# Kernel optimization log

Hardware: AMD Instinct MI355X
Metric: run time of the kernel (lower is better)

The kernel has to match this reference:

```python
import jax, jax.numpy as jnp
import numpy as np

B, N, S, C1, C2 = 8, 8192, 2048, 128, 256
IN_CH = C1 + C2
MLP = [256, 128]
EPS_INTERP = 1e-8
EPS_BN = 1e-5


def setup_inputs() -> dict:
    key = jax.random.key(0)
    ks = jax.random.split(key, 8)
    inp = {
        "xyz1": jax.random.normal(ks[0], (B, 3, N), dtype=jnp.float32),
        "xyz2": jax.random.normal(ks[1], (B, 3, S), dtype=jnp.float32),
        "points1": jax.random.normal(ks[2], (B, C1, N), dtype=jnp.float32),
        "points2": jax.random.normal(ks[3], (B, C2, S), dtype=jnp.float32),
        # Conv1d(k=1) weights as [out, in] matrices, plus BN gamma/beta
        "W1": jax.random.normal(ks[4], (MLP[0], IN_CH), dtype=jnp.float32) * 0.02,
        "b1": jnp.zeros((MLP[0],), dtype=jnp.float32),
        "g1": jnp.ones((MLP[0],), dtype=jnp.float32),
        "be1": jnp.zeros((MLP[0],), dtype=jnp.float32),
        "W2": jax.random.normal(ks[5], (MLP[1], MLP[0]), dtype=jnp.float32) * 0.02,
        "b2": jnp.zeros((MLP[1],), dtype=jnp.float32),
        "g2": jnp.ones((MLP[1],), dtype=jnp.float32),
        "be2": jnp.zeros((MLP[1],), dtype=jnp.float32),
    }
    return inp


def _conv_bn_relu(x, W, b, g, be):
    # x: [B, N, Cin]; 1x1 Conv1d == per-point matmul; BN over (batch, length) per channel (training-mode stats)
    y = jnp.einsum('bnc,oc->bno', x, W) + b
    m = jnp.mean(y, axis=(0, 1))
    v = jnp.var(y, axis=(0, 1))
    return jax.nn.relu((y - m) * jax.lax.rsqrt(v + EPS_BN) * g + be)


def reference(xyz1, xyz2, points1, points2, W1, b1, g1, be1, W2, b2, g2, be2):
    x1 = xyz1.transpose(0, 2, 1)   # [B, N, 3]
    x2 = xyz2.transpose(0, 2, 1)   # [B, S, 3]
    p2 = points2.transpose(0, 2, 1)  # [B, S, C2]
    p1 = points1.transpose(0, 2, 1)  # [B, N, C1]

    # squared pairwise distances [B, N, S]
    d = (jnp.sum(x1 * x1, axis=-1, keepdims=True)
         - 2.0 * jnp.einsum('bnd,bsd->bns', x1, x2)
         + jnp.sum(x2 * x2, axis=-1)[:, None, :])

    # 3 nearest neighbors (smallest distances)
    neg_d, idx = jax.lax.top_k(-d, 3)          # idx: [B, N, 3]
    d3 = -neg_d                                 # [B, N, 3]
    recip = 1.0 / (d3 + EPS_INTERP)
    w = recip / jnp.sum(recip, axis=-1, keepdims=True)  # [B, N, 3]

    gathered = jax.vmap(lambda p, i: p[i])(p2, idx)     # [B, N, 3, C2]
    interp = jnp.sum(gathered * w[..., None], axis=2)   # [B, N, C2]

    x = jnp.concatenate([p1, interp], axis=-1)          # [B, N, C1+C2]
    x = _conv_bn_relu(x, W1, b1, g1, be1)
    x = _conv_bn_relu(x, W2, b2, g2, be2)
    return x.transpose(0, 2, 1)                         # [B, mlp[-1], N]
```

## Files before the change

### kernel.cpp

```cpp
#include <hip/hip_runtime.h>
#include <stdint.h>

#define B_ 8
#define N_ 8192
#define S_ 2048
#define C1_ 128
#define C2_ 256
#define IN_ 384
#define H1_ 256
#define H2_ 128
#define M_ (B_*N_)

typedef short bf16x8 __attribute__((ext_vector_type(8)));
typedef float f32x4 __attribute__((ext_vector_type(4)));

__device__ __forceinline__ float bf2f(unsigned short s){
  union { unsigned int u; float f; } x; x.u = ((unsigned int)s) << 16; return x.f;
}
__device__ __forceinline__ unsigned short f2bf(float f){
  union { float f; unsigned int u; } x; x.f = f;
  unsigned int u = x.u;
  unsigned int r = (u + 0x7FFFu + ((u >> 16) & 1u)) >> 16;
  return (unsigned short)r;
}

__device__ __forceinline__ size_t fragaddr(int m, int k, int K){
  return ((size_t)((m >> 4) * (K >> 5) + (k >> 5)) << 9)
       + (size_t)((((k >> 3) & 3) << 7) + ((m & 15) << 3) + (k & 7));
}

__device__ __forceinline__ void gload_lds16(const unsigned short* g, unsigned short* l){
  __builtin_amdgcn_global_load_lds(
      (const __attribute__((address_space(1))) unsigned int*)g,
      (__attribute__((address_space(3))) unsigned int*)l, 16, 0, 0);
}

#define PIECES_ 8
#define SPP_ (S_ / PIECES_)

__device__ __forceinline__ void insert_k(float& k0, float& k1, float& k2, float x){
  k2 = __builtin_amdgcn_fmed3f(k1, k2, x);
  k1 = __builtin_amdgcn_fmed3f(k0, k1, x);
  k0 = fminf(k0, x);
}

__device__ __forceinline__ void insert3(float& d0, float& d1, float& d2,
                                        int& i0, int& i1, int& i2,
                                        float x, int s){
  bool b0 = x < d0, b1 = x < d1, b2 = x < d2;
  i2 = b1 ? i1 : (b2 ? s : i2);
  i1 = b0 ? i0 : (b1 ? s : i1);
  i0 = b0 ? s : i0;
  d2 = __builtin_amdgcn_fmed3f(d1, d2, x);
  d1 = __builtin_amdgcn_fmed3f(d0, d1, x);
  d0 = fminf(d0, x);
}

__global__ __launch_bounds__(256) void prep_knn_fused(
    const float* W1, const float* W2, const float* p2, const float* p1,
    const float* xyz1, const float* xyz2,
    unsigned short* w1b, unsigned short* w2b, float* stats,
    unsigned short* p2t, unsigned short* x,
    float* partd, int* parti)
{
  __shared__ __align__(16) char smraw[4224];
  float (*tile)[33] = reinterpret_cast<float(*)[33]>(smraw);
  float4* pts = reinterpret_cast<float4*>(smraw);

  const int per = blockIdx.x / 115;
  const int r   = blockIdx.x % 115;
  const int t   = threadIdx.x;

  if (r < 16){
    int kid = per*16 + r;
    int nb = kid & 31, b = (kid >> 5) & 7, piece = kid >> 8;
    int n = nb*256 + t;
    int base = piece * SPP_;
    const float* x2 = xyz2 + (size_t)b * 3 * S_;
    {
      float px = x2[base + t], py = x2[S_ + base + t], pz = x2[2*S_ + base + t];
      pts[t] = make_float4(-2.f*px, -2.f*py, -2.f*pz, px*px + py*py + pz*pz);
    }
    __syncthreads();
    const float* x1 = xyz1 + (size_t)b * 3 * N_;
    float ax = x1[n], ay = x1[N_ + n], az = x1[2*N_ + n];
    float x1sq = ax*ax + ay*ay + az*az;

    const float KINIT = __uint_as_float(0x7F000000u);
    float k[2][3];
    k[0][0]=k[0][1]=k[0][2]=KINIT;
    k[1][0]=k[1][1]=k[1][2]=KINIT;

    for (int s = 0; s < SPP_; s += 8){
      #pragma unroll
      for (int u = 0; u < 8; u++){
        float4 c = pts[s + u];
        float dd = fmaf(ax, c.x, fmaf(ay, c.y, fmaf(az, c.z, c.w + x1sq)));
        float key = __uint_as_float((__float_as_uint(dd) & 0xFFFFFF00u) | (unsigned)(s + u));
        int L = u & 1;
        insert_k(k[L][0], k[L][1], k[L][2], key);
      }
    }
    float e0 = k[0][0], e1 = k[0][1], e2 = k[0][2];
    insert_k(e0, e1, e2, k[1][0]);
    insert_k(e0, e1, e2, k[1][1]);
    insert_k(e0, e1, e2, k[1][2]);

    float ed[3]; int ei[3];
    float ev[3] = {e0, e1, e2};
    #pragma unroll
    for (int j = 0; j < 3; j++){
      int li = (int)(__float_as_uint(ev[j]) & 0xFFu);
      float4 c = pts[li];
      float dd = fmaf(ax, c.x, fmaf(ay, c.y, fmaf(az, c.z, c.w + x1sq)));
      ed[j] = fmaxf(dd, 0.f);
      ei[j] = base + li;
    }

    size_t g = (size_t)b * N_ + n;
    partd[(piece*3 + 0)*(size_t)M_ + g] = ed[0];
    partd[(piece*3 + 1)*(size_t)M_ + g] = ed[1];
    partd[(piece*3 + 2)*(size_t)M_ + g] = ed[2];
    parti[(piece*3 + 0)*(size_t)M_ + g] = ei[0];
    parti[(piece*3 + 1)*(size_t)M_ + g] = ei[1];
    parti[(piece*3 + 2)*(size_t)M_ + g] = ei[2];
    return;
  }

  const int pid = per*99 + (r - 16);
  if (pid < 384){
    int i = pid * 256 + t;
    if (i < 256*384){
      int row = i / 384, col = i - row*384;
      w1b[fragaddr(row, col, 384)] = f2bf(W1[i]);
    }
    if (i < 128*256){
      int row = i >> 8, col = i & 255;
      w2b[fragaddr(row, col, 256)] = f2bf(W2[i]);
    }
    if (i < 1536) stats[i] = 0.f;
    return;
  }
  int tx = t & 31, ty = t >> 5;
  if (pid < 4480){
    int id = pid - 384;
    int b = id >> 9, rem = id & 511;
    int l0 = (rem & 63) * 32, r0 = (rem >> 6) * 32;
    const float* src = p2 + (size_t)b * C2_ * S_;
    #pragma unroll
    for (int rr = ty; rr < 32; rr += 8)
      tile[rr][tx] = src[(size_t)(r0 + rr) * S_ + l0 + tx];
    __syncthreads();
    unsigned short* dst = p2t + (size_t)b * S_ * C2_;
    #pragma unroll
    for (int rr = ty; rr < 32; rr += 8)
      dst[(size_t)(l0 + rr) * C2_ + r0 + tx] = f2bf(tile[tx][rr]);
    return;
  }
  {
    int id = pid - 4480;
    int b = id >> 10, rem = id & 1023;
    int l0 = (rem & 255) * 32, r0 = (rem >> 8) * 32;
    const float* src = p1 + (size_t)b * C1_ * N_;
    #pragma unroll
    for (int rr = ty; rr < 32; rr += 8)
      tile[rr][tx] = src[(size_t)(r0 + rr) * N_ + l0 + tx];
    __syncthreads();
    #pragma unroll
    for (int rr = ty; rr < 32; rr += 8){
      int g = b * N_ + l0 + rr;
      size_t a = ((size_t)((g >> 4)*12 + (r0 >> 5)) << 9)
               + (size_t)((((tx >> 3) & 3) << 7) + ((g & 15) << 3) + (tx & 7));
      x[a] = f2bf(tile[tx][rr]);
    }
  }
}

__global__ __launch_bounds__(256) void interp_kernel(const float* partd, const int* parti,
                                                     const unsigned short* p2t, unsigned short* x){
  __shared__ int   sidx[16][3];
  __shared__ float swgt[16][3];
  int t = threadIdx.x;
  int base = blockIdx.x * 16;
  if (t < 16){
    size_t g = (size_t)base + t;
    float d0 = partd[0*(size_t)M_ + g], d1 = partd[1*(size_t)M_ + g], d2 = partd[2*(size_t)M_ + g];
    int   i0 = parti[0*(size_t)M_ + g], i1 = parti[1*(size_t)M_ + g], i2 = parti[2*(size_t)M_ + g];
    #pragma unroll
    for (int p = 1; p < PIECES_; p++)
      #pragma unroll
      for (int j = 0; j < 3; j++)
        insert3(d0, d1, d2, i0, i1, i2,
                partd[(p*3 + j)*(size_t)M_ + g], parti[(p*3 + j)*(size_t)M_ + g]);
    float r0 = 1.f/(d0 + 1e-8f), r1 = 1.f/(d1 + 1e-8f), r2 = 1.f/(d2 + 1e-8f);
    float rs = 1.f/(r0 + r1 + r2);
    sidx[t][0] = i0; sidx[t][1] = i1; sidx[t][2] = i2;
    swgt[t][0] = r0*rs; swgt[t][1] = r1*rs; swgt[t][2] = r2*rs;
  }
  __syncthreads();
  size_t suboff = (size_t)((((t >> 3) & 3) << 7) + (t & 7));
  for (int k = 0; k < 16; k++){
    int g = base + k;
    int b = g >> 13;
    const unsigned short* p = p2t + (size_t)b * S_ * C2_;
    float v = swgt[k][0]*bf2f(p[(size_t)sidx[k][0]*C2_ + t])
            + swgt[k][1]*bf2f(p[(size_t)sidx[k][1]*C2_ + t])
            + swgt[k][2]*bf2f(p[(size_t)sidx[k][2]*C2_ + t]);
    size_t a = ((size_t)((g >> 4)*12 + 4 + (t >> 5)) << 9) + suboff + (size_t)((g & 15) << 3);
    x[a] = f2bf(v);
  }
}

__device__ __forceinline__ bf16x8 bn_relu_frag(bf16x8 v, const float* a, const float* c, int kb){
  union { bf16x8 h; unsigned short s[8]; } u; u.h = v;
  union { float4 v4; float f[4]; } a0, a1, c0, c1;
  a0.v4 = *(const float4*)(a + kb);  a1.v4 = *(const float4*)(a + kb + 4);
  c0.v4 = *(const float4*)(c + kb);  c1.v4 = *(const float4*)(c + kb + 4);
  #pragma unroll
  for (int j = 0; j < 4; j++){
    float f0 = fmaf(a0.f[j], bf2f(u.s[j]),     c0.f[j]);
    float f1 = fmaf(a1.f[j], bf2f(u.s[j + 4]), c1.f[j]);
    u.s[j]     = f2bf(fmaxf(f0, 0.f));
    u.s[j + 4] = f2bf(fmaxf(f1, 0.f));
  }
  return u.h;
}

template<int K, bool HAS_AFF, bool OUT_FRAG>
__global__ __launch_bounds__(256) void gemm_lds_kernel(
    const unsigned short* __restrict__ A, const unsigned short* __restrict__ Wf,
    unsigned short* __restrict__ Cout, int Ntot,
    float* pbuf, const float* aff_a, const float* aff_c)
{
  constexpr int KT = K / 32;
  __shared__ unsigned short smA[128*64];
  __shared__ unsigned short smB[128*64];
  __shared__ float ldsStat[256];

  const int t = threadIdx.x;
  const int lane = t & 63, wave = t >> 6;
  const int ln = lane & 15, lq = lane >> 4;
  const int wm = wave >> 1, wn = wave & 1;
  const int mtb = blockIdx.x * 8;
  const int ntb = blockIdx.y * 8;
  const int mtw = mtb + wm * 4;
  const int n0  = blockIdx.y * 128 + wn * 64;

  ldsStat[t] = 0.f;

  const int c0 = 2*wave, c1 = 2*wave + 1;

  const f32x4 fzero = {0.f, 0.f, 0.f, 0.f};
  f32x4 acc[4][4];
  #pragma unroll
  for (int i = 0; i < 4; i++)
    #pragma unroll
    for (int j = 0; j < 4; j++) acc[i][j] = fzero;

  for (int kk = 0; kk < KT; kk += 2){
    #pragma unroll
    for (int q = 0; q < 2; q++){
      gload_lds16(A  + (((size_t)((mtb + c0)*KT + kk + q)) << 9) + lane*8,
                  &smA[((c0*2 + q) << 9) + lane*8]);
      gload_lds16(A  + (((size_t)((mtb + c1)*KT + kk + q)) << 9) + lane*8,
                  &smA[((c1*2 + q) << 9) + lane*8]);
      gload_lds16(Wf + (((size_t)((ntb + c0)*KT + kk + q)) << 9) + lane*8,
                  &smB[((c0*2 + q) << 9) + lane*8]);
      gload_lds16(Wf + (((size_t)((ntb + c1)*KT + kk + q)) << 9) + lane*8,
                  &smB[((c1*2 + q) << 9) + lane*8]);
    }
    __syncthreads();
    #pragma unroll
    for (int q = 0; q < 2; q++){
      bf16x8 af[4], bfr[4];
      #pragma unroll
      for (int i = 0; i < 4; i++)
        af[i] = *(const bf16x8*)(&smA[(((wm*4 + i)*2 + q) << 9) + lane*8]);
      #pragma unroll
      for (int j = 0; j < 4; j++)
        bfr[j] = *(const bf16x8*)(&smB[(((wn*4 + j)*2 + q) << 9) + lane*8]);
      if (HAS_AFF){
        const int kb = (kk + q)*32 + lq*8;
        #pragma unroll
        for (int i = 0; i < 4; i++) af[i] = bn_relu_frag(af[i], aff_a, aff_c, kb);
      }
      #pragma unroll
      for (int i = 0; i < 4; i++)
        #pragma unroll
        for (int j = 0; j < 4; j++)
          acc[i][j] = __builtin_amdgcn_mfma_f32_16x16x32_bf16(af[i], bfr[j], acc[i][j], 0, 0, 0);
    }
    __syncthreads();
  }

  #pragma unroll
  for (int j = 0; j < 4; j++){
    int ncol = n0 + j*16 + ln;
    float s = 0.f, q = 0.f;
    #pragma unroll
    for (int i = 0; i < 4; i++){
      #pragma unroll
      for (int r = 0; r < 4; r++){
        float v = acc[i][j][r];
        if (OUT_FRAG){
          size_t a = ((size_t)((mtw + i)*8 + (ncol >> 5)) << 9)
                   + (size_t)((((ncol >> 3) & 3) << 7) + ((lq*4 + r) << 3) + (ncol & 7));
          Cout[a] = f2bf(v);
        } else {
          Cout[((size_t)((mtw + i)*16 + lq*4 + r)) * Ntot + ncol] = f2bf(v);
        }
        s += v; q += v*v;
      }
    }
    s += __shfl_xor(s, 16); s += __shfl_xor(s, 32);
    q += __shfl_xor(q, 16); q += __shfl_xor(q, 32);
    if (lq == 0){
      int colLocal = wn*64 + j*16 + ln;
      atomicAdd(&ldsStat[colLocal], s);
      atomicAdd(&ldsStat[128 + colLocal], q);
    }
  }
  __syncthreads();
  pbuf[((size_t)(blockIdx.y * gridDim.x + blockIdx.x) << 8) + t] = ldsStat[t];
}

__global__ __launch_bounds__(256) void finalize_kernel(const float* pbuf, const float* g,
                                                       const float* be, float* a_out,
                                                       float* c_out){
  __shared__ float red[8];
  int c = blockIdx.x, t = threadIdx.x;
  int grp = c >> 7, lc = c & 127;
  const float* base = pbuf + ((size_t)(grp * 512) << 8);
  float s = base[((size_t)t << 8) + lc]       + base[((size_t)(t + 256) << 8) + lc];
  float q = base[((size_t)t << 8) + 128 + lc] + base[((size_t)(t + 256) << 8) + 128 + lc];
  #pragma unroll
  for (int o = 1; o < 64; o <<= 1){ s += __shfl_xor(s, o); q += __shfl_xor(q, o); }
  int w = t >> 6;
  if ((t & 63) == 0){ red[w] = s; red[4 + w] = q; }
  __syncthreads();
  if (t == 0){
    s = red[0] + red[1] + red[2] + red[3];
    q = red[4] + red[5] + red[6] + red[7];
    float mean = s * (1.f / M_);
    float var  = q * (1.f / M_) - mean*mean;
    float a = g[c] * rsqrtf(var + 1e-5f);
    a_out[c] = a;
    c_out[c] = fmaf(-mean, a, be[c]);
  }
}

__global__ __launch_bounds__(256) void out_kernel(const unsigned short* y2, const float* a2,
                                                  const float* c2, float* out){
  __shared__ float lds[64][65];
  int t  = threadIdx.x;
  int b  = blockIdx.z;
  int n0 = blockIdx.y * 64;
  int c0 = blockIdx.x * 64;
  int cc = t & 63, tr = t >> 6;
  float a = a2[c0 + cc], cadd = c2[c0 + cc];
  #pragma unroll
  for (int ph = 0; ph < 16; ph++){
    int nr = tr + ph*4;
    unsigned short v = y2[((size_t)(b*N_ + n0 + nr)) * H2_ + c0 + cc];
    lds[nr][cc] = fmaxf(fmaf(a, bf2f(v), cadd), 0.f);
  }
  __syncthreads();
  #pragma unroll
  for (int ph = 0; ph < 16; ph++){
    int cr = tr + ph*4;
    out[((size_t)(b*H2_ + c0 + cr)) * N_ + n0 + cc] = lds[cc][cr];
  }
}

extern "C" void kernel_launch(void* const* d_in, const int* in_sizes, int n_in,
                              void* d_out, int out_size, void* d_ws, size_t ws_size,
                              hipStream_t stream){
  const float* xyz1 = (const float*)d_in[0];
  const float* xyz2 = (const float*)d_in[1];
  const float* p1   = (const float*)d_in[2];
  const float* p2   = (const float*)d_in[3];
  const float* W1   = (const float*)d_in[4];
  const float* g1   = (const float*)d_in[6];
  const float* be1  = (const float*)d_in[7];
  const float* W2   = (const float*)d_in[8];
  const float* g2   = (const float*)d_in[10];
  const float* be2  = (const float*)d_in[11];
  float* out = (float*)d_out;

  char* ws = (char*)d_ws;
  unsigned short* x    = (unsigned short*)(ws + 0);
  unsigned short* p2t  = (unsigned short*)(ws + 50331648);
  unsigned short* y1   = (unsigned short*)(ws + 58720256);
  unsigned short* y2   = (unsigned short*)(ws + 92274688);
  unsigned short* w1b  = (unsigned short*)(ws + 109051904);
  unsigned short* w2b  = (unsigned short*)(ws + 109248512);
  float*          stats= (float*)(ws + 110886912);
  float* a1   = stats + 768;  float* c1  = stats + 1024;
  float* a2   = stats + 1280; float* c2  = stats + 1408;
  float* partd = (float*)y1;
  int*   parti = (int*)(y1 + 6291456);
  float* pbuf1 = (float*)p2t;
  float* pbuf2 = (float*)x;

  prep_knn_fused<<<14720, 256, 0, stream>>>(W1, W2, p2, p1, xyz1, xyz2,
                                            w1b, w2b, stats, p2t, x, partd, parti);
  interp_kernel<<<4096, 256, 0, stream>>>(partd, parti, p2t, x);
  gemm_lds_kernel<384, false, true><<<dim3(512, 2), 256, 0, stream>>>(
      x, w1b, y1, 256, pbuf1, nullptr, nullptr);
  finalize_kernel<<<256, 256, 0, stream>>>(pbuf1, g1, be1, a1, c1);
  gemm_lds_kernel<256, true, false><<<dim3(512, 1), 256, 0, stream>>>(
      y1, w2b, y2, 128, pbuf2, a1, c1);
  finalize_kernel<<<128, 256, 0, stream>>>(pbuf2, g2, be2, a2, c2);
  out_kernel<<<dim3(2, 128, 8), 256, 0, stream>>>(y2, a2, c2, out);
}
```

Before: 242.3 us.

## Merge KNN pieces in-block and fuse interpolation with points1 transpose

Each KNN block now walks all S pieces in sequence, staging every piece in LDS. It merges the per-piece top-3 in registers and writes final indices and inverse-distance weights directly, removing the partial distance/index buffers and the separate merge pass. Interpolation and the points1 transpose into the GEMM input layout move into a new build kernel, and the p2 transpose now shares a kernel with KNN and the weight conversion. The aim is to cut global traffic and one launch. The cost is far fewer KNN blocks (one per 256 query points), each serialising all pieces with extra barriers, which lowers parallelism on that stage. The stats zeroing is also dropped.

```diff
diff --git a/kernel.cpp b/kernel.cpp
--- a/kernel.cpp
+++ b/kernel.cpp
@@ -56,96 +56,92 @@
   d0 = fminf(d0, x);
 }
 
-__global__ __launch_bounds__(256) void prep_knn_fused(
-    const float* W1, const float* W2, const float* p2, const float* p1,
+__global__ __launch_bounds__(256) void p2t_knn_kernel(
+    const float* W1, const float* W2, const float* p2,
     const float* xyz1, const float* xyz2,
-    unsigned short* w1b, unsigned short* w2b, float* stats,
-    unsigned short* p2t, unsigned short* x,
-    float* partd, int* parti)
+    unsigned short* w1b, unsigned short* w2b,
+    unsigned short* p2t, int* ibuf, float* wbuf)
 {
-  __shared__ __align__(16) char smraw[4224];
+  __shared__ __align__(16) char smraw[4352];
   float (*tile)[33] = reinterpret_cast<float(*)[33]>(smraw);
   float4* pts = reinterpret_cast<float4*>(smraw);
-
-  const int per = blockIdx.x / 115;
-  const int r   = blockIdx.x % 115;
-  const int t   = threadIdx.x;
-
-  if (r < 16){
-    int kid = per*16 + r;
-    int nb = kid & 31, b = (kid >> 5) & 7, piece = kid >> 8;
-    int n = nb*256 + t;
-    int base = piece * SPP_;
+  const int bx = blockIdx.x, t = threadIdx.x;
+
+  if (bx >= 4352){
+    int i = (bx - 4352) * 256 + t;
+    if (i < 256*384){
+      int row = i / 384, col = i - row*384;
+      w1b[fragaddr(row, col, 384)] = f2bf(W1[i]);
+    }
+    if (i < 128*256){
+      int row = i >> 8, col = i & 255;
+      w2b[fragaddr(row, col, 256)] = f2bf(W2[i]);
+    }
+    return;
+  }
+
+  const int per = bx / 17, r = bx % 17;
+  if (r == 0){
+    int kid = per;
+    int b = kid >> 5, nb = kid & 31;
+    int n = nb * 256 + t;
     const float* x2 = xyz2 + (size_t)b * 3 * S_;
-    {
-      float px = x2[base + t], py = x2[S_ + base + t], pz = x2[2*S_ + base + t];
-      pts[t] = make_float4(-2.f*px, -2.f*py, -2.f*pz, px*px + py*py + pz*pz);
-    }
-    __syncthreads();
     const float* x1 = xyz1 + (size_t)b * 3 * N_;
     float ax = x1[n], ay = x1[N_ + n], az = x1[2*N_ + n];
     float x1sq = ax*ax + ay*ay + az*az;
 
     const float KINIT = __uint_as_float(0x7F000000u);
-    float k[2][3];
-    k[0][0]=k[0][1]=k[0][2]=KINIT;
-    k[1][0]=k[1][1]=k[1][2]=KINIT;
-
-    for (int s = 0; s < SPP_; s += 8){
+    float gd0 = KINIT, gd1 = KINIT, gd2 = KINIT;
+    int   gi0 = 0,     gi1 = 0,     gi2 = 0;
+
+    for (int p = 0; p < PIECES_; p++){
+      int base = p * SPP_;
+      __syncthreads();
+      {
+        float px = x2[base + t], py = x2[S_ + base + t], pz = x2[2*S_ + base + t];
+        pts[t] = make_float4(-2.f*px, -2.f*py, -2.f*pz, px*px + py*py + pz*pz);
+      }
+      __syncthreads();
+      float ka[3] = {KINIT, KINIT, KINIT};
+      float kb[3] = {KINIT, KINIT, KINIT};
+      for (int s = 0; s < SPP_; s += 8){
+        float4 cb[8];
+        #pragma unroll
+        for (int u = 0; u < 8; u++) cb[u] = pts[s + u];
+        #pragma unroll
+        for (int u = 0; u < 8; u++){
+          float dd = fmaf(ax, cb[u].x, fmaf(ay, cb[u].y, fmaf(az, cb[u].z, cb[u].w + x1sq)));
+          float key = __uint_as_float((__float_as_uint(dd) & 0xFFFFFF00u) | (unsigned)(s + u));
+          if (u & 1) insert_k(kb[0], kb[1], kb[2], key);
+          else       insert_k(ka[0], ka[1], ka[2], key);
+        }
+      }
+      insert_k(ka[0], ka[1], ka[2], kb[0]);
+      insert_k(ka[0], ka[1], ka[2], kb[1]);
+      insert_k(ka[0], ka[1], ka[2], kb[2]);
       #pragma unroll
-      for (int u = 0; u < 8; u++){
-        float4 c = pts[s + u];
+      for (int j = 0; j < 3; j++){
+        int li = (int)(__float_as_uint(ka[j]) & 0xFFu);
+        float4 c = pts[li];
         float dd = fmaf(ax, c.x, fmaf(ay, c.y, fmaf(az, c.z, c.w + x1sq)));
-        float key = __uint_as_float((__float_as_uint(dd) & 0xFFFFFF00u) | (unsigned)(s + u));
-        int L = u & 1;
-        insert_k(k[L][0], k[L][1], k[L][2], key);
-      }
-    }
-    float e0 = k[0][0], e1 = k[0][1], e2 = k[0][2];
-    insert_k(e0, e1, e2, k[1][0]);
-    insert_k(e0, e1, e2, k[1][1]);
-    insert_k(e0, e1, e2, k[1][2]);
-
-    float ed[3]; int ei[3];
-    float ev[3] = {e0, e1, e2};
-    #pragma unroll
-    for (int j = 0; j < 3; j++){
-      int li = (int)(__float_as_uint(ev[j]) & 0xFFu);
-      float4 c = pts[li];
-      float dd = fmaf(ax, c.x, fmaf(ay, c.y, fmaf(az, c.z, c.w + x1sq)));
-      ed[j] = fmaxf(dd, 0.f);
-      ei[j] = base + li;
-    }
-
+        dd = fmaxf(dd, 0.f);
+        insert3(gd0, gd1, gd2, gi0, gi1, gi2, dd, base + li);
+      }
+    }
+
+    float r0 = 1.f/(gd0 + 1e-8f), r1 = 1.f/(gd1 + 1e-8f), r2 = 1.f/(gd2 + 1e-8f);
+    float rs = 1.f/(r0 + r1 + r2);
     size_t g = (size_t)b * N_ + n;
-    partd[(piece*3 + 0)*(size_t)M_ + g] = ed[0];
-    partd[(piece*3 + 1)*(size_t)M_ + g] = ed[1];
-    partd[(piece*3 + 2)*(size_t)M_ + g] = ed[2];
-    parti[(piece*3 + 0)*(size_t)M_ + g] = ei[0];
-    parti[(piece*3 + 1)*(size_t)M_ + g] = ei[1];
-    parti[(piece*3 + 2)*(size_t)M_ + g] = ei[2];
+    ibuf[0*(size_t)M_ + g] = gi0; ibuf[1*(size_t)M_ + g] = gi1; ibuf[2*(size_t)M_ + g] = gi2;
+    wbuf[0*(size_t)M_ + g] = r0*rs; wbuf[1*(size_t)M_ + g] = r1*rs; wbuf[2*(size_t)M_ + g] = r2*rs;
     return;
   }
 
-  const int pid = per*99 + (r - 16);
-  if (pid < 384){
-    int i = pid * 256 + t;
-    if (i < 256*384){
-      int row = i / 384, col = i - row*384;
-      w1b[fragaddr(row, col, 384)] = f2bf(W1[i]);
-    }
-    if (i < 128*256){
-      int row = i >> 8, col = i & 255;
-      w2b[fragaddr(row, col, 256)] = f2bf(W2[i]);
-    }
-    if (i < 1536) stats[i] = 0.f;
-    return;
-  }
-  int tx = t & 31, ty = t >> 5;
-  if (pid < 4480){
-    int id = pid - 384;
-    int b = id >> 9, rem = id & 511;
+  {
+    int pid = per*16 + (r - 1);
+    int b = pid >> 9, rem = pid & 511;
     int l0 = (rem & 63) * 32, r0 = (rem >> 6) * 32;
+    int tx = t & 31, ty = t >> 5;
     const float* src = p2 + (size_t)b * C2_ * S_;
     #pragma unroll
     for (int rr = ty; rr < 32; rr += 8)
@@ -155,12 +151,49 @@
     #pragma unroll
     for (int rr = ty; rr < 32; rr += 8)
       dst[(size_t)(l0 + rr) * C2_ + r0 + tx] = f2bf(tile[tx][rr]);
+  }
+}
+
+__global__ __launch_bounds__(256) void xbuild_kernel(
+    const float* p1, const unsigned short* p2t,
+    const int* ibuf, const float* wbuf, unsigned short* x)
+{
+  __shared__ __align__(16) char smraw[4352];
+  float (*tile)[33] = reinterpret_cast<float(*)[33]>(smraw);
+  int*   sidx = reinterpret_cast<int*>(smraw);
+  float* swgt = reinterpret_cast<float*>(smraw + 192);
+  const int bx = blockIdx.x, t = threadIdx.x;
+  const int per = bx / 3, r = bx % 3;
+
+  if (r == 0){
+    int base = per * 16;
+    if (t < 64){
+      int q = t >> 2, j = t & 3;
+      if (j < 3){
+        sidx[q*3 + j] = ibuf[(size_t)j*M_ + base + q];
+        swgt[q*3 + j] = wbuf[(size_t)j*M_ + base + q];
+      }
+    }
+    __syncthreads();
+    size_t suboff = (size_t)((((t >> 3) & 3) << 7) + (t & 7));
+    for (int k = 0; k < 16; k++){
+      int g = base + k;
+      int b = g >> 13;
+      const unsigned short* p = p2t + (size_t)b * S_ * C2_;
+      float v = swgt[k*3+0]*bf2f(p[(size_t)sidx[k*3+0]*C2_ + t])
+              + swgt[k*3+1]*bf2f(p[(size_t)sidx[k*3+1]*C2_ + t])
+              + swgt[k*3+2]*bf2f(p[(size_t)sidx[k*3+2]*C2_ + t]);
+      size_t a = ((size_t)((g >> 4)*12 + 4 + (t >> 5)) << 9) + suboff + (size_t)((g & 15) << 3);
+      x[a] = f2bf(v);
+    }
     return;
   }
+
   {
-    int id = pid - 4480;
-    int b = id >> 10, rem = id & 1023;
+    int pid = per*2 + (r - 1);
+    int b = pid >> 10, rem = pid & 1023;
     int l0 = (rem & 255) * 32, r0 = (rem >> 8) * 32;
+    int tx = t & 31, ty = t >> 5;
     const float* src = p1 + (size_t)b * C1_ * N_;
     #pragma unroll
     for (int rr = ty; rr < 32; rr += 8)
@@ -173,41 +206,6 @@
                + (size_t)((((tx >> 3) & 3) << 7) + ((g & 15) << 3) + (tx & 7));
       x[a] = f2bf(tile[tx][rr]);
     }
-  }
-}
-
-__global__ __launch_bounds__(256) void interp_kernel(const float* partd, const int* parti,
-                                                     const unsigned short* p2t, unsigned short* x){
-  __shared__ int   sidx[16][3];
-  __shared__ float swgt[16][3];
-  int t = threadIdx.x;
-  int base = blockIdx.x * 16;
-  if (t < 16){
-    size_t g = (size_t)base + t;
-    float d0 = partd[0*(size_t)M_ + g], d1 = partd[1*(size_t)M_ + g], d2 = partd[2*(size_t)M_ + g];
-    int   i0 = parti[0*(size_t)M_ + g], i1 = parti[1*(size_t)M_ + g], i2 = parti[2*(size_t)M_ + g];
-    #pragma unroll
-    for (int p = 1; p < PIECES_; p++)
-      #pragma unroll
-      for (int j = 0; j < 3; j++)
-        insert3(d0, d1, d2, i0, i1, i2,
-                partd[(p*3 + j)*(size_t)M_ + g], parti[(p*3 + j)*(size_t)M_ + g]);
-    float r0 = 1.f/(d0 + 1e-8f), r1 = 1.f/(d1 + 1e-8f), r2 = 1.f/(d2 + 1e-8f);
-    float rs = 1.f/(r0 + r1 + r2);
-    sidx[t][0] = i0; sidx[t][1] = i1; sidx[t][2] = i2;
-    swgt[t][0] = r0*rs; swgt[t][1] = r1*rs; swgt[t][2] = r2*rs;
-  }
-  __syncthreads();
-  size_t suboff = (size_t)((((t >> 3) & 3) << 7) + (t & 7));
-  for (int k = 0; k < 16; k++){
-    int g = base + k;
-    int b = g >> 13;
-    const unsigned short* p = p2t + (size_t)b * S_ * C2_;
-    float v = swgt[k][0]*bf2f(p[(size_t)sidx[k][0]*C2_ + t])
-            + swgt[k][1]*bf2f(p[(size_t)sidx[k][1]*C2_ + t])
-            + swgt[k][2]*bf2f(p[(size_t)sidx[k][2]*C2_ + t]);
-    size_t a = ((size_t)((g >> 4)*12 + 4 + (t >> 5)) << 9) + suboff + (size_t)((g & 15) << 3);
-    x[a] = f2bf(v);
   }
 }
 
@@ -397,14 +395,13 @@
   float*          stats= (float*)(ws + 110886912);
   float* a1   = stats + 768;  float* c1  = stats + 1024;
   float* a2   = stats + 1280; float* c2  = stats + 1408;
-  float* partd = (float*)y1;
-  int*   parti = (int*)(y1 + 6291456);
+  int*   ibuf = (int*)y1;
+  float* wbuf = (float*)(ws + 58720256 + 0x100000);
   float* pbuf1 = (float*)p2t;
   float* pbuf2 = (float*)x;
 
-  prep_knn_fused<<<14720, 256, 0, stream>>>(W1, W2, p2, p1, xyz1, xyz2,
-                                            w1b, w2b, stats, p2t, x, partd, parti);
-  interp_kernel<<<4096, 256, 0, stream>>>(partd, parti, p2t, x);
+  p2t_knn_kernel<<<4736, 256, 0, stream>>>(W1, W2, p2, xyz1, xyz2, w1b, w2b, p2t, ibuf, wbuf);
+  xbuild_kernel<<<12288, 256, 0, stream>>>(p1, p2t, ibuf, wbuf, x);
   gemm_lds_kernel<384, false, true><<<dim3(512, 2), 256, 0, stream>>>(
       x, w1b, y1, 256, pbuf1, nullptr, nullptr);
   finalize_kernel<<<256, 256, 0, stream>>>(pbuf1, g1, be1, a1, c1);
```

New measurement: 294.3 us. +21.5%, slower.

## Split interpolation into parallel merge kernel and vectorized gather kernel

Applied to the files above, without the earlier changes.

The combined interp kernel merged per-piece top-3 candidates using only 16 threads per block, so 240 of 256 threads sat idle during the merge. The merge now runs as its own kernel with one thread per point and writes indices and weights to a workspace buffer. A separate gather kernel loads 4 bf16 channels per lane with vector loads, puts one wave on each point, and writes 8-byte stores. This costs an extra kernel launch and a round trip of the index and weight arrays through global memory.

```diff
diff --git a/kernel.cpp b/kernel.cpp
--- a/kernel.cpp
+++ b/kernel.cpp
@@ -13,6 +13,8 @@
 
 typedef short bf16x8 __attribute__((ext_vector_type(8)));
 typedef float f32x4 __attribute__((ext_vector_type(4)));
+typedef short short4v __attribute__((ext_vector_type(4)));
+typedef unsigned short ushort4v __attribute__((ext_vector_type(4)));
 
 __device__ __forceinline__ float bf2f(unsigned short s){
   union { unsigned int u; float f; } x; x.u = ((unsigned int)s) << 16; return x.f;
@@ -176,38 +178,64 @@
   }
 }
 
-__global__ __launch_bounds__(256) void interp_kernel(const float* partd, const int* parti,
-                                                     const unsigned short* p2t, unsigned short* x){
-  __shared__ int   sidx[16][3];
-  __shared__ float swgt[16][3];
-  int t = threadIdx.x;
+__global__ __launch_bounds__(256) void merge_kernel(const float* __restrict__ partd,
+                                                    const int* __restrict__ parti,
+                                                    int* __restrict__ ibuf,
+                                                    float* __restrict__ wbuf){
+  size_t g = (size_t)blockIdx.x * 256 + threadIdx.x;
+  float d0 = partd[0*(size_t)M_ + g], d1 = partd[1*(size_t)M_ + g], d2 = partd[2*(size_t)M_ + g];
+  int   i0 = parti[0*(size_t)M_ + g], i1 = parti[1*(size_t)M_ + g], i2 = parti[2*(size_t)M_ + g];
+  #pragma unroll
+  for (int p = 1; p < PIECES_; p++)
+    #pragma unroll
+    for (int j = 0; j < 3; j++)
+      insert3(d0, d1, d2, i0, i1, i2,
+              partd[(p*3 + j)*(size_t)M_ + g], parti[(p*3 + j)*(size_t)M_ + g]);
+  float r0 = 1.f/(d0 + 1e-8f), r1 = 1.f/(d1 + 1e-8f), r2 = 1.f/(d2 + 1e-8f);
+  float rs = 1.f/(r0 + r1 + r2);
+  ibuf[0*(size_t)M_ + g] = i0;    ibuf[1*(size_t)M_ + g] = i1;    ibuf[2*(size_t)M_ + g] = i2;
+  wbuf[0*(size_t)M_ + g] = r0*rs; wbuf[1*(size_t)M_ + g] = r1*rs; wbuf[2*(size_t)M_ + g] = r2*rs;
+}
+
+__global__ __launch_bounds__(256) void gather_kernel(
+    const unsigned short* __restrict__ p2t, const int* __restrict__ ibuf,
+    const float* __restrict__ wbuf, unsigned short* __restrict__ x)
+{
+  __shared__ int   sidx[48];
+  __shared__ float swgt[48];
+  const int t = threadIdx.x;
   int base = blockIdx.x * 16;
-  if (t < 16){
-    size_t g = (size_t)base + t;
-    float d0 = partd[0*(size_t)M_ + g], d1 = partd[1*(size_t)M_ + g], d2 = partd[2*(size_t)M_ + g];
-    int   i0 = parti[0*(size_t)M_ + g], i1 = parti[1*(size_t)M_ + g], i2 = parti[2*(size_t)M_ + g];
-    #pragma unroll
-    for (int p = 1; p < PIECES_; p++)
-      #pragma unroll
-      for (int j = 0; j < 3; j++)
-        insert3(d0, d1, d2, i0, i1, i2,
-                partd[(p*3 + j)*(size_t)M_ + g], parti[(p*3 + j)*(size_t)M_ + g]);
-    float r0 = 1.f/(d0 + 1e-8f), r1 = 1.f/(d1 + 1e-8f), r2 = 1.f/(d2 + 1e-8f);
-    float rs = 1.f/(r0 + r1 + r2);
-    sidx[t][0] = i0; sidx[t][1] = i1; sidx[t][2] = i2;
-    swgt[t][0] = r0*rs; swgt[t][1] = r1*rs; swgt[t][2] = r2*rs;
+  if (t < 64){
+    int q = t >> 2, j = t & 3;
+    if (j < 3){
+      sidx[q*3 + j] = ibuf[(size_t)j*M_ + base + q];
+      swgt[q*3 + j] = wbuf[(size_t)j*M_ + base + q];
+    }
   }
   __syncthreads();
-  size_t suboff = (size_t)((((t >> 3) & 3) << 7) + (t & 7));
-  for (int k = 0; k < 16; k++){
+  const int wv = t >> 6, ln = t & 63;
+  #pragma unroll
+  for (int kq = 0; kq < 4; kq++){
+    int k = kq*4 + wv;
     int g = base + k;
     int b = g >> 13;
     const unsigned short* p = p2t + (size_t)b * S_ * C2_;
-    float v = swgt[k][0]*bf2f(p[(size_t)sidx[k][0]*C2_ + t])
-            + swgt[k][1]*bf2f(p[(size_t)sidx[k][1]*C2_ + t])
-            + swgt[k][2]*bf2f(p[(size_t)sidx[k][2]*C2_ + t]);
-    size_t a = ((size_t)((g >> 4)*12 + 4 + (t >> 5)) << 9) + suboff + (size_t)((g & 15) << 3);
-    x[a] = f2bf(v);
+    float a0 = 0.f, a1 = 0.f, a2 = 0.f, a3 = 0.f;
+    #pragma unroll
+    for (int j = 0; j < 3; j++){
+      ushort4v v = *(const ushort4v*)(p + (size_t)sidx[k*3+j]*C2_ + 4*ln);
+      float w = swgt[k*3+j];
+      a0 = fmaf(w, bf2f(v[0]), a0);
+      a1 = fmaf(w, bf2f(v[1]), a1);
+      a2 = fmaf(w, bf2f(v[2]), a2);
+      a3 = fmaf(w, bf2f(v[3]), a3);
+    }
+    short4v o;
+    o[0] = (short)f2bf(a0); o[1] = (short)f2bf(a1);
+    o[2] = (short)f2bf(a2); o[3] = (short)f2bf(a3);
+    size_t a = ((size_t)((g >> 4)*12 + 4 + (ln >> 3)) << 9)
+             + (size_t)((((ln >> 1) & 3) << 7) + ((g & 15) << 3) + ((ln & 1) * 4));
+    *(short4v*)(x + a) = o;
   }
 }
 
@@ -399,12 +427,15 @@
   float* a2   = stats + 1280; float* c2  = stats + 1408;
   float* partd = (float*)y1;
   int*   parti = (int*)(y1 + 6291456);
+  int*   ibuf = (int*)  (ws + 58720256 + 20971520);
+  float* wbuf = (float*)(ws + 58720256 + 23068672);
   float* pbuf1 = (float*)p2t;
   float* pbuf2 = (float*)x;
 
   prep_knn_fused<<<14720, 256, 0, stream>>>(W1, W2, p2, p1, xyz1, xyz2,
                                             w1b, w2b, stats, p2t, x, partd, parti);
-  interp_kernel<<<4096, 256, 0, stream>>>(partd, parti, p2t, x);
+  merge_kernel<<<256, 256, 0, stream>>>(partd, parti, ibuf, wbuf);
+  gather_kernel<<<4096, 256, 0, stream>>>(p2t, ibuf, wbuf, x);
   gemm_lds_kernel<384, false, true><<<dim3(512, 2), 256, 0, stream>>>(
       x, w1b, y1, 256, pbuf1, nullptr, nullptr);
   finalize_kernel<<<256, 256, 0, stream>>>(pbuf1, g1, be1, a1, c1);
```

Result: no change. 242.9 us (+0.3%).
